# Performance work log

Measured on AMD Instinct MI355X. Metric: run time of the kernel, lower is better.

## Reference

```python
import jax, jax.numpy as jnp
import numpy as np

DIM = 256; QK = 256; HEADS = 8; TOPK = 2; WV = 2; WH = 2
SCALE = QK ** -0.5


def setup_inputs() -> dict:
    key = jax.random.key(0)
    ks = jax.random.split(key, 6)
    x = jax.random.normal(ks[0], (4, DIM, 64, 64), jnp.float32)
    Wqkv = jax.random.normal(ks[1], (DIM, 2 * QK + DIM), jnp.float32) * 0.02
    bqkv = jnp.zeros((2 * QK + DIM,), jnp.float32)
    Wo = jax.random.normal(ks[2], (DIM, DIM), jnp.float32) * 0.02
    bo = jnp.zeros((DIM,), jnp.float32)
    lepe_w = jax.random.normal(ks[3], (3, 3, 1, DIM), jnp.float32) * 0.1  # HWIO depthwise
    lepe_b = jnp.zeros((DIM,), jnp.float32)
    return {"x": x, "Wqkv": Wqkv, "bqkv": bqkv, "Wo": Wo, "bo": bo,
            "lepe_w": lepe_w, "lepe_b": lepe_b}


def _dwconv(x, w, b):
    # depthwise 3x3 conv, NHWC
    y = jax.lax.conv_general_dilated(x, w, (1, 1), 'SAME',
                                     dimension_numbers=('NHWC', 'HWIO', 'NHWC'),
                                     feature_group_count=x.shape[-1])
    return y + b


def _branch(win, Wqkv, bqkv, lepe_w, lepe_b, to_image):
    n, p2, h, w, _ = win.shape
    w2 = h * w
    qkv = win @ Wqkv + bqkv
    q = qkv[..., :QK]
    kv = qkv[..., QK:]                                  # [n,p2,h,w,QK+DIM]
    q_pix = q.reshape(n, p2, w2, QK)
    kv_pix = kv.reshape(n, p2, w2, QK + DIM)            # identity kv_down
    # region routing (detached in original)
    q_win = jax.lax.stop_gradient(q).mean((2, 3))       # [n,p2,QK]
    k_win = jax.lax.stop_gradient(kv[..., :QK]).mean((2, 3))
    logit = jnp.einsum('npc,nqc->npq', q_win * SCALE, k_win)
    _, r_idx = jax.lax.top_k(logit, TOPK)               # [n,p2,TOPK]
    # gather selected KV windows (mul_weight='none')
    kv_sel = jax.vmap(lambda kvb, idxb: kvb[idxb])(kv_pix, r_idx)  # [n,p2,k,w2,ckv]
    k_sel = kv_sel[..., :QK].reshape(n, p2, TOPK * w2, HEADS, QK // HEADS)
    v_sel = kv_sel[..., QK:].reshape(n, p2, TOPK * w2, HEADS, DIM // HEADS)
    qh = q_pix.reshape(n, p2, w2, HEADS, QK // HEADS)
    attn = jax.nn.softmax(jnp.einsum('npqhd,npkhd->nphqk', qh * SCALE, k_sel), axis=-1)
    out = jnp.einsum('nphqk,npkhd->npqhd', attn, v_sel).reshape(n, p2, h, w, DIM)
    lepe = _dwconv(to_image(kv[..., QK:]), lepe_w, lepe_b)
    return to_image(out) + lepe


def reference(x, Wqkv, bqkv, Wo, bo, lepe_w, lepe_b):
    xh = x.transpose(0, 2, 3, 1)                        # NHWC
    N, H, W, C = xh.shape
    v_win, h_win = H // WV, W // WH
    # vertical branch: horizontal strips of height WV, full width
    vm = xh.reshape(N, v_win, WV, W, C)
    # horizontal branch: vertical strips of width WH, full height
    hm = xh.reshape(N, H, h_win, WH, C).transpose(0, 2, 1, 3, 4)
    img_v = lambda a: a.reshape(N, H, W, a.shape[-1])
    img_h = lambda a: a.transpose(0, 2, 1, 3, 4).reshape(N, H, W, a.shape[-1])
    o1 = _branch(vm, Wqkv, bqkv, lepe_w, lepe_b, img_v)
    o2 = _branch(hm, Wqkv, bqkv, lepe_w, lepe_b, img_h)
    out = (o1 @ Wo + bo) + (o2 @ Wo + bo)
    return out.transpose(0, 3, 1, 2)                    # back to NCHW
```

## Files before the change

kernel.cpp:

```cpp
#include <hip/hip_runtime.h>
#include <hip/hip_bf16.h>
#include <math.h>

#define NBATCH 4
#define HW     4096
#define NPIX   16384
#define SCALE  0.0625f
#define QLOG2E (0.0625f * 1.44269504088896340736f)

typedef __attribute__((ext_vector_type(8))) short bf16x8;
typedef __attribute__((ext_vector_type(4))) float f32x4;

__device__ __forceinline__ int pixmap(int b, int n, int p, int pos){
  return (b == 0) ? (n*HW + p*128 + pos)
                  : (n*HW + (pos >> 1)*64 + (p << 1) + (pos & 1));
}

__device__ __forceinline__ ushort f2b(float x){
  __hip_bfloat16 h = __float2bfloat16(x);
  return *reinterpret_cast<ushort*>(&h);
}
__device__ __forceinline__ float b2f(ushort u){
  __hip_bfloat16 h = *reinterpret_cast<__hip_bfloat16*>(&u);
  return __bfloat162float(h);
}
__device__ __forceinline__ uint pk2(float a, float b){
  return (uint)f2b(a) | ((uint)f2b(b) << 16);
}

__global__ __launch_bounds__(256) void k_xt(
    const float* __restrict__ x, ushort* __restrict__ Xb)
{
  __shared__ float T[32][257];
  const int n = blockIdx.y, hw0 = blockIdx.x * 32;
  const int tid = threadIdx.x;
  const int hl = tid & 31, cg = tid >> 5;
  #pragma unroll 8
  for(int i = 0; i < 32; i++){
    const int c = i*8 + cg;
    T[hl][c] = x[((size_t)(n*256 + c))*4096 + hw0 + hl];
  }
  __syncthreads();
  const int c0 = (tid & 31)*8, pb = tid >> 5;
  #pragma unroll
  for(int i = 0; i < 4; i++){
    const int p = pb + 8*i;
    union { bf16x8 v; ushort u[8]; } U;
    #pragma unroll
    for(int j = 0; j < 8; j++) U.u[j] = f2b(T[p][c0 + j]);
    *(bf16x8*)(Xb + ((size_t)(n*HW + hw0 + p))*256 + c0) = U.v;
  }
}

__global__ __launch_bounds__(256) void k_wt(
    const float* __restrict__ Wqkv, ushort* __restrict__ Wt)
{
  const int o = blockIdx.x, t = threadIdx.x;
  Wt[(size_t)o*256 + t] = f2b(Wqkv[(size_t)t*768 + o]);
}

__global__ __launch_bounds__(256) void k_wto(
    const float* __restrict__ Wo, ushort* __restrict__ WoT)
{
  const int o = blockIdx.x, t = threadIdx.x;
  WoT[(size_t)o*256 + t] = f2b(Wo[(size_t)t*256 + o]);
}

__global__ __launch_bounds__(256) void k_qkv_mfma(
    const ushort* __restrict__ Xb, const ushort* __restrict__ Wt,
    const float* __restrict__ bqkv, ushort* __restrict__ QKVb)
{
  const int tid = threadIdx.x;
  const int l = tid & 63, w = tid >> 6;
  const int wr = w >> 1, wc = w & 1;
  const int q16 = l & 15, g = l >> 4;
  const int row0 = blockIdx.x*128 + wr*64;
  const int col0 = blockIdx.y*128 + wc*64;

  f32x4 acc[4][4];
  #pragma unroll
  for(int i = 0; i < 4; i++)
    #pragma unroll
    for(int j = 0; j < 4; j++) acc[i][j] = (f32x4){0,0,0,0};

  const ushort* Ab = Xb + (size_t)(row0 + q16)*256 + 8*g;
  const ushort* Bb = Wt + (size_t)(col0 + q16)*256 + 8*g;

  #pragma unroll
  for(int ks = 0; ks < 8; ks++){
    const int k0 = ks*32;
    bf16x8 a[4], b[4];
    #pragma unroll
    for(int i = 0; i < 4; i++) a[i] = *(const bf16x8*)(Ab + (size_t)(16*i)*256 + k0);
    #pragma unroll
    for(int j = 0; j < 4; j++) b[j] = *(const bf16x8*)(Bb + (size_t)(16*j)*256 + k0);
    #pragma unroll
    for(int i = 0; i < 4; i++)
      #pragma unroll
      for(int j = 0; j < 4; j++)
        acc[i][j] = __builtin_amdgcn_mfma_f32_16x16x32_bf16(a[i], b[j], acc[i][j], 0, 0, 0);
  }

  #pragma unroll
  for(int j = 0; j < 4; j++){
    const int col = col0 + 16*j + q16;
    const float bias = bqkv[col];
    const float sc = (col < 256) ? QLOG2E : 1.f;
    #pragma unroll
    for(int i = 0; i < 4; i++){
      #pragma unroll
      for(int r = 0; r < 4; r++){
        const int row = row0 + 16*i + 4*g + r;
        QKVb[(size_t)row*768 + col] = f2b((acc[i][j][r] + bias) * sc);
      }
    }
  }
}

__global__ __launch_bounds__(256) void k_vt(
    const ushort* __restrict__ QKVb, ushort* __restrict__ Vt)
{
  __shared__ ushort T[32][258];
  const int tile = blockIdx.x;
  const int n = tile >> 7;
  const int hw0 = (tile & 127) * 32;
  const int tid = threadIdx.x;
  #pragma unroll 4
  for(int i = 0; i < 32; i++)
    T[i][tid] = QKVb[(size_t)(n*HW + hw0 + i)*768 + 512 + tid];
  __syncthreads();
  const int px = tid & 31, wv = tid >> 5;
  #pragma unroll 4
  for(int ccb = 0; ccb < 32; ccb++){
    const int c = ccb*8 + wv;
    Vt[((size_t)(n*256 + c))*4096 + hw0 + px] = T[px][c];
  }
}

__global__ __launch_bounds__(256) void k_xmean(
    const float* __restrict__ x, float* __restrict__ xwin)
{
  const int n = blockIdx.y;
  const int c = blockIdx.x*4 + (threadIdx.x >> 6);
  const int l = threadIdx.x & 63;
  const float* xc = x + ((size_t)(n*256 + c))*4096;

  float4 cs[8];
  #pragma unroll
  for(int i = 0; i < 8; i++) cs[i] = (float4){0,0,0,0};
  float rsum = 0.f;
  const float4* xr = (const float4*)(xc + l*64);
  #pragma unroll
  for(int i = 0; i < 16; i++){
    const float4 v = xr[i];
    rsum += (v.x+v.y)+(v.z+v.w);
    const float p0 = v.x+v.y, p1 = v.z+v.w;
    if(i & 1){ cs[i>>1].z += p0; cs[i>>1].w += p1; }
    else     { cs[i>>1].x += p0; cs[i>>1].y += p1; }
  }
  #pragma unroll
  for(int i = 0; i < 8; i++){
    #pragma unroll
    for(int s = 1; s < 64; s <<= 1){
      cs[i].x += __shfl_xor(cs[i].x, s);
      cs[i].y += __shfl_xor(cs[i].y, s);
      cs[i].z += __shfl_xor(cs[i].z, s);
      cs[i].w += __shfl_xor(cs[i].w, s);
    }
  }
  const int p = l & 31;
  const float rp = __shfl(rsum, 2*p) + __shfl(rsum, 2*p + 1);
  float cp;
  {
    const int hi = p >> 2, lo = p & 3;
    const float4 q = hi==0?cs[0]:hi==1?cs[1]:hi==2?cs[2]:hi==3?cs[3]
                   : hi==4?cs[4]:hi==5?cs[5]:hi==6?cs[6]:cs[7];
    cp = lo==0?q.x : lo==1?q.y : lo==2?q.z : q.w;
  }
  if(l < 32){
    xwin[((size_t)((0*NBATCH + n)*32 + p))*256 + c] = rp * (1.f/128.f);
    xwin[((size_t)((1*NBATCH + n)*32 + p))*256 + c] = cp * (1.f/128.f);
  }
}

__global__ __launch_bounds__(256) void k_win_gemm(
    const float* __restrict__ xwin, const float* __restrict__ Wqkv,
    const float* __restrict__ bqkv, float* __restrict__ qwin, float* __restrict__ kwin)
{
  __shared__ float xs[256];
  const int row = blockIdx.x;
  const int tid = threadIdx.x;
  xs[tid] = xwin[(size_t)row*256 + tid];
  __syncthreads();
  #pragma unroll
  for(int half = 0; half < 2; half++){
    const int col = half*256 + tid;
    float s = 0.f;
    for(int k = 0; k < 256; k++) s += xs[k] * Wqkv[(size_t)k*768 + col];
    s += bqkv[col];
    if(half == 0) qwin[(size_t)row*256 + tid] = s;
    else          kwin[(size_t)row*256 + tid] = s;
  }
}

__global__ __launch_bounds__(256) void k_logits_top2(
    const float* __restrict__ qwin, const float* __restrict__ kwin, int* __restrict__ ridx)
{
  const int n = blockIdx.x, b = blockIdx.y;
  __shared__ float lg[32][32];
  const int base = ((b*NBATCH + n)*32)*256;
  for(int t = threadIdx.x; t < 1024; t += 256){
    const int p = t >> 5, q = t & 31;
    const float* qp = qwin + base + p*256;
    const float* kq = kwin + base + q*256;
    float s = 0.f;
    for(int c = 0; c < 256; c++) s += qp[c]*kq[c];
    lg[p][q] = s * SCALE;
  }
  __syncthreads();
  if(threadIdx.x < 32){
    const int p = threadIdx.x;
    float m0 = -INFINITY; int i0 = 0;
    for(int q = 0; q < 32; q++){ const float v = lg[p][q]; if(v > m0){ m0 = v; i0 = q; } }
    float m1 = -INFINITY; int i1 = 0;
    for(int q = 0; q < 32; q++){ if(q == i0) continue; const float v = lg[p][q]; if(v > m1){ m1 = v; i1 = q; } }
    const int o = ((b*NBATCH + n)*32 + p)*2;
    ridx[o] = i0; ridx[o+1] = i1;
  }
}

__global__ __launch_bounds__(256) void k_attn_mfma(
    const ushort* __restrict__ QKVb, const ushort* __restrict__ Vt,
    const int* __restrict__ ridx, ushort* __restrict__ Ob)
{
  int id = blockIdx.x*4 + (threadIdx.x >> 6);
  const int hd = id & 7;  id >>= 3;
  const int p  = id & 31; id >>= 5;
  const int n  = id & 3;  id >>= 2;
  const int b  = id;
  const int l = threadIdx.x & 63;
  const int q16 = l & 15, g = l >> 4;

  const int ro = ((b*NBATCH + n)*32 + p)*2;
  const int r0 = ridx[ro], r1 = ridx[ro+1];

  int qpix[8];
  bf16x8 qf[8];
  #pragma unroll
  for(int m = 0; m < 8; m++){
    qpix[m] = pixmap(b, n, p, m*16 + q16);
    qf[m] = *(const bf16x8*)(QKVb + (size_t)qpix[m]*768 + hd*32 + 8*g);
  }

  f32x4 acc0[8], acc1[8];
  float rs[8];
  #pragma unroll
  for(int m = 0; m < 8; m++){
    acc0[m] = (f32x4){0,0,0,0}; acc1[m] = (f32x4){0,0,0,0}; rs[m] = 0.f;
  }

  for(int c = 0; c < 8; c++){
    const int wsel = (c < 4) ? r0 : r1;
    const int posb = (32*c) & 127;

    bf16x8 kf0, kf1;
    {
      const int kp0 = pixmap(b, n, wsel, posb + q16);
      kf0 = *(const bf16x8*)(QKVb + (size_t)kp0*768 + 256 + hd*32 + 8*g);
      const int kp1 = pixmap(b, n, wsel, posb + 16 + q16);
      kf1 = *(const bf16x8*)(QKVb + (size_t)kp1*768 + 256 + hd*32 + 8*g);
    }
    bf16x8 vf0, vf1;
    if(b == 0){
      const ushort* base = Vt + ((size_t)(n*256 + hd*32 + q16))*4096 + wsel*128 + posb + 4*g;
      union { bf16x8 v; ushort4 h[2]; } U0, U1;
      U0.h[0] = *(const ushort4*)(base);
      U0.h[1] = *(const ushort4*)(base + 16);
      U1.h[0] = *(const ushort4*)(base + (size_t)16*4096);
      U1.h[1] = *(const ushort4*)(base + (size_t)16*4096 + 16);
      vf0 = U0.v; vf1 = U1.v;
    } else {
      const int h0 = (posb + 4*g) >> 1;
      const ushort* base = Vt + ((size_t)(n*256 + hd*32 + q16))*4096 + 2*wsel;
      union { bf16x8 v; uint u[4]; } U0, U1;
      U0.u[0] = *(const uint*)(base + (h0    )*64);
      U0.u[1] = *(const uint*)(base + (h0 + 1)*64);
      U0.u[2] = *(const uint*)(base + (h0 + 8)*64);
      U0.u[3] = *(const uint*)(base + (h0 + 9)*64);
      const ushort* base1 = base + (size_t)16*4096;
      U1.u[0] = *(const uint*)(base1 + (h0    )*64);
      U1.u[1] = *(const uint*)(base1 + (h0 + 1)*64);
      U1.u[2] = *(const uint*)(base1 + (h0 + 8)*64);
      U1.u[3] = *(const uint*)(base1 + (h0 + 9)*64);
      vf0 = U0.v; vf1 = U1.v;
    }

    #pragma unroll
    for(int m = 0; m < 8; m++){
      const f32x4 z = {0,0,0,0};
      f32x4 s0 = __builtin_amdgcn_mfma_f32_16x16x32_bf16(kf0, qf[m], z, 0, 0, 0);
      f32x4 s1 = __builtin_amdgcn_mfma_f32_16x16x32_bf16(kf1, qf[m], z, 0, 0, 0);
      const float e00 = exp2f(s0[0]), e01 = exp2f(s0[1]), e02 = exp2f(s0[2]), e03 = exp2f(s0[3]);
      const float e10 = exp2f(s1[0]), e11 = exp2f(s1[1]), e12 = exp2f(s1[2]), e13 = exp2f(s1[3]);
      rs[m] += ((e00+e01)+(e02+e03)) + ((e10+e11)+(e12+e13));
      union { bf16x8 v; uint u[4]; } P;
      P.u[0] = pk2(e00, e01);
      P.u[1] = pk2(e02, e03);
      P.u[2] = pk2(e10, e11);
      P.u[3] = pk2(e12, e13);
      acc0[m] = __builtin_amdgcn_mfma_f32_16x16x32_bf16(vf0, P.v, acc0[m], 0, 0, 0);
      acc1[m] = __builtin_amdgcn_mfma_f32_16x16x32_bf16(vf1, P.v, acc1[m], 0, 0, 0);
    }
  }

  #pragma unroll
  for(int m = 0; m < 8; m++){
    float r = rs[m];
    r += __shfl_xor(r, 16);
    r += __shfl_xor(r, 32);
    rs[m] = 1.f / r;
  }
  #pragma unroll
  for(int m = 0; m < 8; m++){
    ushort* op = Ob + ((size_t)b*NPIX + qpix[m])*256 + hd*32 + 4*g;
    const float iv = rs[m];
    ushort4 o0 = { f2b(acc0[m][0]*iv), f2b(acc0[m][1]*iv), f2b(acc0[m][2]*iv), f2b(acc0[m][3]*iv) };
    ushort4 o1 = { f2b(acc1[m][0]*iv), f2b(acc1[m][1]*iv), f2b(acc1[m][2]*iv), f2b(acc1[m][3]*iv) };
    *(ushort4*)op = o0;
    *(ushort4*)(op + 16) = o1;
  }
}

__global__ __launch_bounds__(256) void k_combine_lepe(
    const ushort* __restrict__ QKVb, const ushort* __restrict__ Ob0,
    const ushort* __restrict__ Ob1,
    const float* __restrict__ lw, const float* __restrict__ lb, ushort* __restrict__ Sb)
{
  const int pix = blockIdx.x;
  const int c = threadIdx.x;
  const int n = pix >> 12, rem = pix & 4095;
  const int h = rem >> 6, w = rem & 63;
  float conv = 0.f;
  #pragma unroll
  for(int kh = 0; kh < 3; kh++){
    const int hh = h + kh - 1;
    if(hh < 0 || hh >= 64) continue;
    #pragma unroll
    for(int kw = 0; kw < 3; kw++){
      const int wi = w + kw - 1;
      if(wi < 0 || wi >= 64) continue;
      const int np = (n*64 + hh)*64 + wi;
      conv += b2f(QKVb[(size_t)np*768 + 512 + c]) * lw[(kh*3 + kw)*256 + c];
    }
  }
  const size_t idx = (size_t)pix*256 + c;
  Sb[idx] = f2b(b2f(Ob0[idx]) + b2f(Ob1[idx]) + 2.f*(conv + lb[c]));
}

__global__ __launch_bounds__(256) void k_out_mfma(
    const ushort* __restrict__ Sb, const ushort* __restrict__ WoT,
    const float* __restrict__ bo, float* __restrict__ out)
{
  const int tid = threadIdx.x;
  const int l = tid & 63, w = tid >> 6;
  const int wr = w >> 1, wc = w & 1;
  const int q16 = l & 15, g = l >> 4;
  const int c0   = blockIdx.x*128 + wr*64;
  const int pix0 = blockIdx.y*128 + wc*64;
  const int n = pix0 >> 12, rem0 = pix0 & 4095;

  f32x4 acc[4][4];
  #pragma unroll
  for(int i = 0; i < 4; i++)
    #pragma unroll
    for(int j = 0; j < 4; j++) acc[i][j] = (f32x4){0,0,0,0};

  const ushort* Ab = WoT + (size_t)(c0 + q16)*256 + 8*g;
  const ushort* Bb = Sb  + (size_t)(pix0 + q16)*256 + 8*g;

  #pragma unroll
  for(int ks = 0; ks < 8; ks++){
    const int k0 = ks*32;
    bf16x8 a[4], b[4];
    #pragma unroll
    for(int i = 0; i < 4; i++) a[i] = *(const bf16x8*)(Ab + (size_t)(16*i)*256 + k0);
    #pragma unroll
    for(int j = 0; j < 4; j++) b[j] = *(const bf16x8*)(Bb + (size_t)(16*j)*256 + k0);
    #pragma unroll
    for(int i = 0; i < 4; i++)
      #pragma unroll
      for(int j = 0; j < 4; j++)
        acc[i][j] = __builtin_amdgcn_mfma_f32_16x16x32_bf16(a[i], b[j], acc[i][j], 0, 0, 0);
  }

  float* outn = out + (size_t)n*256*4096;
  #pragma unroll
  for(int i = 0; i < 4; i++){
    #pragma unroll
    for(int r = 0; r < 4; r++){
      const int c = c0 + 16*i + 4*g + r;
      const float bias = 2.f*bo[c];
      #pragma unroll
      for(int j = 0; j < 4; j++){
        const int rem = rem0 + 16*j + q16;
        outn[(size_t)c*4096 + rem] = acc[i][j][r] + bias;
      }
    }
  }
}

extern "C" void kernel_launch(void* const* d_in, const int* in_sizes, int n_in,
                              void* d_out, int out_size, void* d_ws, size_t ws_size,
                              hipStream_t stream)
{
  const float* x    = (const float*)d_in[0];
  const float* Wqkv = (const float*)d_in[1];
  const float* bqkv = (const float*)d_in[2];
  const float* Wo   = (const float*)d_in[3];
  const float* bo   = (const float*)d_in[4];
  const float* lw   = (const float*)d_in[5];
  const float* lb   = (const float*)d_in[6];
  float* out = (float*)d_out;

  char* w = (char*)d_ws;
  ushort* Xb   = (ushort*)w; w += (size_t)NPIX*256*2;
  ushort* Wt   = (ushort*)w; w += (size_t)768*256*2;
  ushort* WoT  = (ushort*)w; w += (size_t)256*256*2;
  ushort* QKVb = (ushort*)w; w += (size_t)NPIX*768*2;
  ushort* Vt   = (ushort*)w; w += (size_t)NPIX*256*2;
  ushort* Ob   = (ushort*)w; w += (size_t)2*NPIX*256*2;
  ushort* Sb   = (ushort*)w; w += (size_t)NPIX*256*2;
  float*  xwin = (float*)w;  w += (size_t)2*NBATCH*32*256*4;
  float*  qwin = (float*)w;  w += (size_t)2*NBATCH*32*256*4;
  float*  kwin = (float*)w;  w += (size_t)2*NBATCH*32*256*4;
  int*    ridx = (int*)w;    w += (size_t)2*NBATCH*32*2*4;

  ushort* Ob0 = Ob;
  ushort* Ob1 = Ob + (size_t)NPIX*256;

  k_xt          <<<dim3(128,NBATCH), 256, 0, stream>>>(x, Xb);
  k_wt          <<<768, 256, 0, stream>>>(Wqkv, Wt);
  k_wto         <<<256, 256, 0, stream>>>(Wo, WoT);
  k_qkv_mfma    <<<dim3(128,6), 256, 0, stream>>>(Xb, Wt, bqkv, QKVb);
  k_vt          <<<512, 256, 0, stream>>>(QKVb, Vt);
  k_xmean       <<<dim3(64,NBATCH), 256, 0, stream>>>(x, xwin);
  k_win_gemm    <<<256, 256, 0, stream>>>(xwin, Wqkv, bqkv, qwin, kwin);
  k_logits_top2 <<<dim3(NBATCH,2), 256, 0, stream>>>(qwin, kwin, ridx);
  k_attn_mfma   <<<512, 256, 0, stream>>>(QKVb, Vt, ridx, Ob);
  k_combine_lepe<<<NPIX, 256, 0, stream>>>(QKVb, Ob0, Ob1, lw, lb, Sb);
  k_out_mfma    <<<dim3(2,128), 256, 0, stream>>>(Sb, WoT, bo, out);
}
```

Measured before the change: 190.3 us.

## Fuse V transpose into QKV GEMM epilogue and split attention query rows

The QKV GEMM epilogue now writes the V columns directly in the transposed Vt layout with ushort4 stores, so the separate k_vt transpose kernel and its extra read of QKVb are removed. The attention kernel also splits each window's 128 query rows across two waves, doubling the grid to 1024 blocks. This is meant to raise parallelism and cut register pressure per wave. The cost is that K/V fragments are loaded twice, once by each wave.

```diff
diff --git a/kernel.cpp b/kernel.cpp
--- a/kernel.cpp
+++ b/kernel.cpp
@@ -68,7 +68,8 @@
 
 __global__ __launch_bounds__(256) void k_qkv_mfma(
     const ushort* __restrict__ Xb, const ushort* __restrict__ Wt,
-    const float* __restrict__ bqkv, ushort* __restrict__ QKVb)
+    const float* __restrict__ bqkv, ushort* __restrict__ QKVb,
+    ushort* __restrict__ Vt)
 {
   const int tid = threadIdx.x;
   const int l = tid & 63, w = tid >> 6;
@@ -101,6 +102,7 @@
         acc[i][j] = __builtin_amdgcn_mfma_f32_16x16x32_bf16(a[i], b[j], acc[i][j], 0, 0, 0);
   }
 
+  const int n = row0 >> 12, hwb = row0 & 4095;
   #pragma unroll
   for(int j = 0; j < 4; j++){
     const int col = col0 + 16*j + q16;
@@ -108,32 +110,20 @@
     const float sc = (col < 256) ? QLOG2E : 1.f;
     #pragma unroll
     for(int i = 0; i < 4; i++){
-      #pragma unroll
-      for(int r = 0; r < 4; r++){
-        const int row = row0 + 16*i + 4*g + r;
-        QKVb[(size_t)row*768 + col] = f2b((acc[i][j][r] + bias) * sc);
+      ushort4 u;
+      u.x = f2b((acc[i][j][0] + bias) * sc);
+      u.y = f2b((acc[i][j][1] + bias) * sc);
+      u.z = f2b((acc[i][j][2] + bias) * sc);
+      u.w = f2b((acc[i][j][3] + bias) * sc);
+      const int row = row0 + 16*i + 4*g;
+      QKVb[(size_t)(row+0)*768 + col] = u.x;
+      QKVb[(size_t)(row+1)*768 + col] = u.y;
+      QKVb[(size_t)(row+2)*768 + col] = u.z;
+      QKVb[(size_t)(row+3)*768 + col] = u.w;
+      if(col >= 512){
+        *(ushort4*)&Vt[((size_t)(n*256 + col - 512))*4096 + hwb + 16*i + 4*g] = u;
       }
     }
-  }
-}
-
-__global__ __launch_bounds__(256) void k_vt(
-    const ushort* __restrict__ QKVb, ushort* __restrict__ Vt)
-{
-  __shared__ ushort T[32][258];
-  const int tile = blockIdx.x;
-  const int n = tile >> 7;
-  const int hw0 = (tile & 127) * 32;
-  const int tid = threadIdx.x;
-  #pragma unroll 4
-  for(int i = 0; i < 32; i++)
-    T[i][tid] = QKVb[(size_t)(n*HW + hw0 + i)*768 + 512 + tid];
-  __syncthreads();
-  const int px = tid & 31, wv = tid >> 5;
-  #pragma unroll 4
-  for(int ccb = 0; ccb < 32; ccb++){
-    const int c = ccb*8 + wv;
-    Vt[((size_t)(n*256 + c))*4096 + hw0 + px] = T[px][c];
   }
 }
 
@@ -234,6 +224,7 @@
     const int* __restrict__ ridx, ushort* __restrict__ Ob)
 {
   int id = blockIdx.x*4 + (threadIdx.x >> 6);
+  const int half = id & 1; id >>= 1;
   const int hd = id & 7;  id >>= 3;
   const int p  = id & 31; id >>= 5;
   const int n  = id & 3;  id >>= 2;
@@ -244,18 +235,18 @@
   const int ro = ((b*NBATCH + n)*32 + p)*2;
   const int r0 = ridx[ro], r1 = ridx[ro+1];
 
-  int qpix[8];
-  bf16x8 qf[8];
-  #pragma unroll
-  for(int m = 0; m < 8; m++){
-    qpix[m] = pixmap(b, n, p, m*16 + q16);
+  int qpix[4];
+  bf16x8 qf[4];
+  #pragma unroll
+  for(int m = 0; m < 4; m++){
+    qpix[m] = pixmap(b, n, p, (half*4 + m)*16 + q16);
     qf[m] = *(const bf16x8*)(QKVb + (size_t)qpix[m]*768 + hd*32 + 8*g);
   }
 
-  f32x4 acc0[8], acc1[8];
-  float rs[8];
-  #pragma unroll
-  for(int m = 0; m < 8; m++){
+  f32x4 acc0[4], acc1[4];
+  float rs[4];
+  #pragma unroll
+  for(int m = 0; m < 4; m++){
     acc0[m] = (f32x4){0,0,0,0}; acc1[m] = (f32x4){0,0,0,0}; rs[m] = 0.f;
   }
 
@@ -296,7 +287,7 @@
     }
 
     #pragma unroll
-    for(int m = 0; m < 8; m++){
+    for(int m = 0; m < 4; m++){
       const f32x4 z = {0,0,0,0};
       f32x4 s0 = __builtin_amdgcn_mfma_f32_16x16x32_bf16(kf0, qf[m], z, 0, 0, 0);
       f32x4 s1 = __builtin_amdgcn_mfma_f32_16x16x32_bf16(kf1, qf[m], z, 0, 0, 0);
@@ -314,14 +305,14 @@
   }
 
   #pragma unroll
-  for(int m = 0; m < 8; m++){
+  for(int m = 0; m < 4; m++){
     float r = rs[m];
     r += __shfl_xor(r, 16);
     r += __shfl_xor(r, 32);
     rs[m] = 1.f / r;
   }
   #pragma unroll
-  for(int m = 0; m < 8; m++){
+  for(int m = 0; m < 4; m++){
     ushort* op = Ob + ((size_t)b*NPIX + qpix[m])*256 + hd*32 + 4*g;
     const float iv = rs[m];
     ushort4 o0 = { f2b(acc0[m][0]*iv), f2b(acc0[m][1]*iv), f2b(acc0[m][2]*iv), f2b(acc0[m][3]*iv) };
@@ -441,12 +432,11 @@
   k_xt          <<<dim3(128,NBATCH), 256, 0, stream>>>(x, Xb);
   k_wt          <<<768, 256, 0, stream>>>(Wqkv, Wt);
   k_wto         <<<256, 256, 0, stream>>>(Wo, WoT);
-  k_qkv_mfma    <<<dim3(128,6), 256, 0, stream>>>(Xb, Wt, bqkv, QKVb);
-  k_vt          <<<512, 256, 0, stream>>>(QKVb, Vt);
+  k_qkv_mfma    <<<dim3(128,6), 256, 0, stream>>>(Xb, Wt, bqkv, QKVb, Vt);
   k_xmean       <<<dim3(64,NBATCH), 256, 0, stream>>>(x, xwin);
   k_win_gemm    <<<256, 256, 0, stream>>>(xwin, Wqkv, bqkv, qwin, kwin);
   k_logits_top2 <<<dim3(NBATCH,2), 256, 0, stream>>>(qwin, kwin, ridx);
-  k_attn_mfma   <<<512, 256, 0, stream>>>(QKVb, Vt, ridx, Ob);
+  k_attn_mfma   <<<1024, 256, 0, stream>>>(QKVb, Vt, ridx, Ob);
   k_combine_lepe<<<NPIX, 256, 0, stream>>>(QKVb, Ob0, Ob1, lw, lb, Sb);
   k_out_mfma    <<<dim3(2,128), 256, 0, stream>>>(Sb, WoT, bo, out);
 }
```

Result: slower. 208.6 us (+9.6%).
